# Kernel optimization log

Hardware: AMD Instinct MI355X
Metric: run time of the kernel (lower is better)

Reference implementation:

```python
import jax, jax.numpy as jnp
import numpy as np

N, D_MODEL, D_PE, H = 4096, 512, 16, 8


def setup_inputs() -> dict:
    key = jax.random.key(0)
    ks = jax.random.split(key, 6)
    s = 1.0 / np.sqrt(D_MODEL)
    return {
        "x": jax.random.normal(ks[0], (N, D_MODEL), dtype=jnp.float32),
        "pe": jax.random.normal(ks[1], (N, D_PE), dtype=jnp.float32),
        "w_qkv": jax.random.normal(ks[2], (D_MODEL, 3 * D_MODEL), dtype=jnp.float32) * s,
        "b_qkv": jnp.zeros((3 * D_MODEL,), dtype=jnp.float32),
        "w_pe": jax.random.normal(ks[3], (D_PE, H), dtype=jnp.float32) * (1.0 / np.sqrt(D_PE)),
        "b_pe": jnp.zeros((H,), dtype=jnp.float32),
        "w_out": jax.random.normal(ks[4], (D_MODEL, D_MODEL), dtype=jnp.float32) * s,
        "b_out": jnp.zeros((D_MODEL,), dtype=jnp.float32),
    }


def reference(x, pe, w_qkv, b_qkv, w_pe, b_pe, w_out, b_out):
    n, d = x.shape
    h = w_pe.shape[1]
    hd = d // h
    scale = hd ** -0.5

    qkv = (x @ w_qkv + b_qkv).reshape(n, 3, h, hd)  # [N,3,H,hd]
    q = jnp.transpose(qkv[:, 0], (1, 0, 2))  # [H,N,hd]
    k = jnp.transpose(qkv[:, 1], (1, 0, 2))
    v = jnp.transpose(qkv[:, 2], (1, 0, 2))

    pe_proj = pe @ w_pe + b_pe  # [N,H]
    # bias[h,i,j] = pe_proj[j,h] - pe_proj[i,h]  (matches torch unsqueeze/permute)
    pt = pe_proj.T  # [H,N]
    bias = pt[:, None, :] - pt[:, :, None]  # [H,N,N]

    scores = jnp.einsum('hnd,hmd->hnm', q, k) * scale + bias  # [H,N,N]
    attn = jax.nn.softmax(scores, axis=-1)
    out = jnp.einsum('hnm,hmd->hnd', attn, v)  # [H,N,hd]
    out = jnp.transpose(out, (1, 0, 2)).reshape(n, d)
    return out @ w_out + b_out
```

## Files before the change

### kernel.cpp

```cpp
#include <hip/hip_runtime.h>
#include <stdint.h>
#include <stddef.h>


typedef unsigned short u16;
typedef __attribute__((ext_vector_type(8))) short short8;
typedef __attribute__((ext_vector_type(8))) unsigned short us8;
typedef __attribute__((ext_vector_type(4))) unsigned short us4;
typedef __attribute__((ext_vector_type(4))) float floatx4;

__device__ __forceinline__ u16 f2b(float f) {
  union { float f; uint32_t u; } v; v.f = f;
  uint32_t u = v.u;
  return (u16)((u + 0x7fffu + ((u >> 16) & 1u)) >> 16);
}

__device__ __forceinline__ uint32_t pkbf16(float a, float b) {
  union { float f; uint32_t u; } x, y; x.f = a; y.f = b;
  return __builtin_amdgcn_perm(y.u + 0x8000u, x.u + 0x8000u, 0x07060302u);
}

#if __has_builtin(__builtin_amdgcn_exp2f)
__device__ __forceinline__ float fexp2(float x) { return __builtin_amdgcn_exp2f(x); }
#else
__device__ __forceinline__ float fexp2(float x) { return exp2f(x); }
#endif


__device__ __forceinline__ void tr_tile(const float* __restrict__ in,
                                        u16* __restrict__ out, int R, int C,
                                        int bx, int by, u16 (*tile)[33]) {
  int tx = threadIdx.x & 31, ty = threadIdx.x >> 5;
  int c0 = bx * 32, r0 = by * 32;
#pragma unroll
  for (int i = 0; i < 32; i += 8)
    tile[ty + i][tx] = f2b(in[(size_t)(r0 + ty + i) * C + c0 + tx]);
  __syncthreads();
#pragma unroll
  for (int i = 0; i < 32; i += 8)
    out[(size_t)(c0 + ty + i) * R + r0 + tx] = tile[tx][ty + i];
}

__global__ __launch_bounds__(256) void k_prep(
    const float* __restrict__ x, u16* __restrict__ xb,
    const float* __restrict__ w_qkv, u16* __restrict__ wqkvT,
    const float* __restrict__ w_out, u16* __restrict__ woutT,
    const float* __restrict__ pe, const float* __restrict__ w_pe,
    const float* __restrict__ b_pe, float* __restrict__ peT) {
  __shared__ u16 tile[32][33];
  int b = blockIdx.x;
  if (b < 2048) {
    int i = b * 256 + threadIdx.x;
    float4 v = ((const float4*)x)[i];
    uint2 o = make_uint2(pkbf16(v.x, v.y), pkbf16(v.z, v.w));
    ((uint2*)xb)[i] = o;
  } else if (b < 2816) {
    int idx = b - 2048;
    tr_tile(w_qkv, wqkvT, 512, 1536, idx % 48, idx / 48, tile);
  } else if (b < 3072) {
    int idx = b - 2816;
    tr_tile(w_out, woutT, 512, 512, idx % 16, idx / 16, tile);
  } else {
    int idx = (b - 3072) * 256 + threadIdx.x;
    int h = idx >> 12, n = idx & 4095;
    float acc = b_pe[h];
#pragma unroll
    for (int d = 0; d < 16; ++d) acc = fmaf(pe[n * 16 + d], w_pe[d * 8 + h], acc);
    peT[h * 4096 + n] = acc * 1.4426950408889634f - 16.0f;
  }
}


__global__ __launch_bounds__(256) void k_gemm_qkv(const u16* __restrict__ A,
                                                  const u16* __restrict__ Bt,
                                                  const float* __restrict__ bias,
                                                  u16* __restrict__ qk,
                                                  u16* __restrict__ vtp) {
  __shared__ u16 As[64 * 40];
  __shared__ u16 Bs[128 * 40];
  const int tid = threadIdx.x;
  const int lane = tid & 63, wave = tid >> 6;
  const int colx = lane & 15, quad = lane >> 4;
  const int m0 = blockIdx.y * 64, n0 = blockIdx.x * 128;
  const int wr = (wave >> 1) * 32, wc = (wave & 1) * 64;
  const floatx4 fz = {0.f, 0.f, 0.f, 0.f};
  floatx4 acc[2][4];
#pragma unroll
  for (int i = 0; i < 2; ++i)
#pragma unroll
    for (int j = 0; j < 4; ++j) acc[i][j] = fz;

  for (int k0 = 0; k0 < 512; k0 += 32) {
    __syncthreads();
    {
      int row = tid >> 2, ch = tid & 3;
      *(us8*)&As[row * 40 + ch * 8] =
          *(const us8*)&A[(size_t)(m0 + row) * 512 + k0 + ch * 8];
    }
#pragma unroll
    for (int r = 0; r < 2; ++r) {
      int idx = r * 256 + tid;
      int row = idx >> 2, ch = idx & 3;
      *(us8*)&Bs[row * 40 + ch * 8] =
          *(const us8*)&Bt[(size_t)(n0 + row) * 512 + k0 + ch * 8];
    }
    __syncthreads();
    short8 af[2], bf[4];
#pragma unroll
    for (int i = 0; i < 2; ++i)
      af[i] = *(const short8*)&As[(wr + i * 16 + colx) * 40 + quad * 8];
#pragma unroll
    for (int j = 0; j < 4; ++j)
      bf[j] = *(const short8*)&Bs[(wc + j * 16 + colx) * 40 + quad * 8];
#pragma unroll
    for (int i = 0; i < 2; ++i)
#pragma unroll
      for (int j = 0; j < 4; ++j)
        acc[i][j] = __builtin_amdgcn_mfma_f32_16x16x32_bf16(af[i], bf[j], acc[i][j], 0, 0, 0);
  }

  const bool isV = (blockIdx.x >= 8);
#pragma unroll
  for (int j = 0; j < 4; ++j) {
    int c = n0 + wc + j * 16 + colx;
    float bq = bias[c];
    if (!isV) {
#pragma unroll
      for (int i = 0; i < 2; ++i)
#pragma unroll
        for (int r = 0; r < 4; ++r) {
          int row = m0 + wr + i * 16 + quad * 4 + r;
          qk[(size_t)row * 1024 + c] = f2b(acc[i][j][r] + bq);
        }
    } else {
      int d = c - 1024;
#pragma unroll
      for (int i = 0; i < 2; ++i) {
        us4 o;
#pragma unroll
        for (int r = 0; r < 4; ++r) o[r] = f2b(acc[i][j][r] + bq);
        *(us4*)&vtp[(size_t)d * 4096 + m0 + wr + quad * 8 + i * 4] = o;
      }
    }
  }
}


__global__ __launch_bounds__(256) void k_gemm_out(const u16* __restrict__ A,
                                                  const u16* __restrict__ Bt,
                                                  const float* __restrict__ bias,
                                                  float* __restrict__ Cout) {
  __shared__ u16 As[64 * 40];
  __shared__ u16 Bs[64 * 40];
  const int tid = threadIdx.x;
  const int lane = tid & 63, wave = tid >> 6;
  const int colx = lane & 15, quad = lane >> 4;
  const int m0 = blockIdx.y * 64, n0 = blockIdx.x * 64;
  const int wr = (wave >> 1) * 32, wc = (wave & 1) * 32;
  const floatx4 fz = {0.f, 0.f, 0.f, 0.f};
  floatx4 acc[2][2];
#pragma unroll
  for (int i = 0; i < 2; ++i)
#pragma unroll
    for (int j = 0; j < 2; ++j) acc[i][j] = fz;

  for (int k0 = 0; k0 < 512; k0 += 32) {
    __syncthreads();
    {
      int row = tid >> 2, ch = tid & 3;
      *(us8*)&As[row * 40 + ch * 8] =
          *(const us8*)&A[(size_t)(m0 + row) * 512 + k0 + ch * 8];
      *(us8*)&Bs[row * 40 + ch * 8] =
          *(const us8*)&Bt[(size_t)(n0 + row) * 512 + k0 + ch * 8];
    }
    __syncthreads();
    short8 af[2], bf[2];
#pragma unroll
    for (int i = 0; i < 2; ++i)
      af[i] = *(const short8*)&As[(wr + i * 16 + colx) * 40 + quad * 8];
#pragma unroll
    for (int j = 0; j < 2; ++j)
      bf[j] = *(const short8*)&Bs[(wc + j * 16 + colx) * 40 + quad * 8];
#pragma unroll
    for (int i = 0; i < 2; ++i)
#pragma unroll
      for (int j = 0; j < 2; ++j)
        acc[i][j] = __builtin_amdgcn_mfma_f32_16x16x32_bf16(af[i], bf[j], acc[i][j], 0, 0, 0);
  }
#pragma unroll
  for (int j = 0; j < 2; ++j) {
    int c = n0 + wc + j * 16 + colx;
    float bq = bias[c];
#pragma unroll
    for (int i = 0; i < 2; ++i)
#pragma unroll
      for (int r = 0; r < 4; ++r) {
        int row = m0 + wr + i * 16 + quad * 4 + r;
        Cout[(size_t)row * 512 + c] = acc[i][j][r] + bq;
      }
  }
}


__global__ __launch_bounds__(512, 4) void k_flash(const u16* __restrict__ qk,
                                                  const u16* __restrict__ vt,
                                                  const float* __restrict__ peT,
                                                  u16* __restrict__ ao) {
  __shared__ __align__(16) u16 smem[18176];
  u16* Ks = smem;
  u16* Vts = smem + 9216;
  float* pes = (float*)(smem + 17920);
  float* bufs = (float*)smem;
  u16* fin = smem;

  const int tid = threadIdx.x;
  const int lane = tid & 63, wave = tid >> 6;
  const int colx = lane & 15, quad = lane >> 4;
  const int ih = wave & 1, jq = wave >> 1;
  const int q0 = blockIdx.x * 64;
  const int h = blockIdx.y;
  const float sscale = 0.125f * 1.4426950408889634f;
  const floatx4 fz = {0.f, 0.f, 0.f, 0.f};

  {
    int row = tid >> 3, ch = tid & 7;
    *(us8*)&Ks[row * 72 + ch * 8] =
        *(const us8*)&qk[(size_t)(q0 + row) * 1024 + h * 64 + ch * 8];
  }
  __syncthreads();
  short8 qf[2][2];
#pragma unroll
  for (int i2 = 0; i2 < 2; ++i2)
#pragma unroll
    for (int kk = 0; kk < 2; ++kk)
      qf[i2][kk] = *(const short8*)&Ks[(ih * 32 + i2 * 16 + colx) * 72 + kk * 32 + quad * 8];

  floatx4 oacc[2][4];
  float rsum[2] = {0.0f, 0.0f};
#pragma unroll
  for (int i2 = 0; i2 < 2; ++i2)
#pragma unroll
    for (int cb = 0; cb < 4; ++cb) oacc[i2][cb] = fz;

  for (int j0 = 0; j0 < 4096; j0 += 128) {
    __syncthreads();
#pragma unroll
    for (int r = 0; r < 2; ++r) {
      int idx = r * 512 + tid;
      int row = idx >> 3, ch = idx & 7;
      *(us8*)&Ks[row * 72 + ch * 8] =
          *(const us8*)&qk[(size_t)(j0 + row) * 1024 + 512 + h * 64 + ch * 8];
    }
#pragma unroll
    for (int r = 0; r < 2; ++r) {
      int idx = r * 512 + tid;
      int row = idx >> 4, ch = idx & 15;
      *(us8*)&Vts[row * 136 + ch * 8] =
          *(const us8*)&vt[(size_t)(h * 64 + row) * 4096 + j0 + ch * 8];
    }
    if (tid < 128) pes[tid] = peT[h * 4096 + j0 + tid];
    __syncthreads();

    short8 kf[2][2];
#pragma unroll
    for (int j2 = 0; j2 < 2; ++j2)
#pragma unroll
      for (int kk = 0; kk < 2; ++kk)
        kf[j2][kk] = *(const short8*)&Ks[(jq * 32 + j2 * 16 + colx) * 72 + kk * 32 + quad * 8];
    short8 vf[4];
#pragma unroll
    for (int cb = 0; cb < 4; ++cb)
      vf[cb] = *(const short8*)&Vts[(cb * 16 + colx) * 136 + jq * 32 + quad * 8];
    floatx4 pev[2];
#pragma unroll
    for (int j2 = 0; j2 < 2; ++j2)
      pev[j2] = *(const floatx4*)&pes[jq * 32 + j2 * 16 + quad * 4];

#pragma unroll
    for (int i2 = 0; i2 < 2; ++i2) {
      floatx4 sacc[2] = {fz, fz};
#pragma unroll
      for (int j2 = 0; j2 < 2; ++j2)
#pragma unroll
        for (int kk = 0; kk < 2; ++kk)
          sacc[j2] = __builtin_amdgcn_mfma_f32_16x16x32_bf16(kf[j2][kk], qf[i2][kk], sacc[j2], 0, 0, 0);
      union { uint32_t w[4]; short8 s; } pk;
#pragma unroll
      for (int j2 = 0; j2 < 2; ++j2) {
        float p0 = fexp2(fmaf(sacc[j2][0], sscale, pev[j2][0]));
        float p1 = fexp2(fmaf(sacc[j2][1], sscale, pev[j2][1]));
        float p2 = fexp2(fmaf(sacc[j2][2], sscale, pev[j2][2]));
        float p3 = fexp2(fmaf(sacc[j2][3], sscale, pev[j2][3]));
        rsum[i2] += (p0 + p1) + (p2 + p3);
        pk.w[j2 * 2 + 0] = pkbf16(p0, p1);
        pk.w[j2 * 2 + 1] = pkbf16(p2, p3);
      }
#pragma unroll
      for (int cb = 0; cb < 4; ++cb)
        oacc[i2][cb] = __builtin_amdgcn_mfma_f32_16x16x32_bf16(pk.s, vf[cb], oacc[i2][cb], 0, 0, 0);
    }
  }

  floatx4 lacc[2];
#pragma unroll
  for (int i2 = 0; i2 < 2; ++i2) {
    rsum[i2] += __shfl_xor(rsum[i2], 16);
    rsum[i2] += __shfl_xor(rsum[i2], 32);
#pragma unroll
    for (int r = 0; r < 4; ++r) lacc[i2][r] = __shfl(rsum[i2], quad * 4 + r, 16);
  }

  __syncthreads();
  float* s0 = bufs + (0 * 2 + ih) * 2080;
  float* s1 = bufs + (1 * 2 + ih) * 2080;
  if (jq >= 2) {
    float* b = (jq == 2) ? s0 : s1;
#pragma unroll
    for (int i2 = 0; i2 < 2; ++i2) {
#pragma unroll
      for (int cb = 0; cb < 4; ++cb)
#pragma unroll
        for (int r = 0; r < 4; ++r)
          b[(i2 * 16 + quad * 4 + r) * 65 + cb * 16 + colx] = oacc[i2][cb][r];
      if (colx == 0)
#pragma unroll
        for (int r = 0; r < 4; ++r)
          b[(i2 * 16 + quad * 4 + r) * 65 + 64] = lacc[i2][r];
    }
  }
  __syncthreads();
  if (jq < 2) {
    float* b = (jq == 0) ? s0 : s1;
#pragma unroll
    for (int i2 = 0; i2 < 2; ++i2) {
#pragma unroll
      for (int cb = 0; cb < 4; ++cb)
#pragma unroll
        for (int r = 0; r < 4; ++r)
          oacc[i2][cb][r] += b[(i2 * 16 + quad * 4 + r) * 65 + cb * 16 + colx];
#pragma unroll
      for (int r = 0; r < 4; ++r)
        lacc[i2][r] += b[(i2 * 16 + quad * 4 + r) * 65 + 64];
    }
  }
  __syncthreads();
  if (jq == 1) {
#pragma unroll
    for (int i2 = 0; i2 < 2; ++i2) {
#pragma unroll
      for (int cb = 0; cb < 4; ++cb)
#pragma unroll
        for (int r = 0; r < 4; ++r)
          s1[(i2 * 16 + quad * 4 + r) * 65 + cb * 16 + colx] = oacc[i2][cb][r];
      if (colx == 0)
#pragma unroll
        for (int r = 0; r < 4; ++r)
          s1[(i2 * 16 + quad * 4 + r) * 65 + 64] = lacc[i2][r];
    }
  }
  __syncthreads();
  if (jq == 0) {
#pragma unroll
    for (int i2 = 0; i2 < 2; ++i2) {
#pragma unroll
      for (int cb = 0; cb < 4; ++cb)
#pragma unroll
        for (int r = 0; r < 4; ++r)
          oacc[i2][cb][r] += s1[(i2 * 16 + quad * 4 + r) * 65 + cb * 16 + colx];
#pragma unroll
      for (int r = 0; r < 4; ++r)
        lacc[i2][r] += s1[(i2 * 16 + quad * 4 + r) * 65 + 64];
#pragma unroll
      for (int r = 0; r < 4; ++r) {
        float inv = 1.0f / lacc[i2][r];
#pragma unroll
        for (int cb = 0; cb < 4; ++cb)
          fin[(ih * 32 + i2 * 16 + quad * 4 + r) * 68 + cb * 16 + colx] =
              f2b(oacc[i2][cb][r] * inv);
      }
    }
  }
  __syncthreads();
  {
    int row = tid >> 3, ch = tid & 7;
    *(us8*)&ao[(size_t)(q0 + row) * 512 + h * 64 + ch * 8] =
        *(const us8*)&fin[row * 68 + ch * 8];
  }
}


extern "C" void kernel_launch(void* const* d_in, const int* in_sizes, int n_in,
                              void* d_out, int out_size, void* d_ws, size_t ws_size,
                              hipStream_t stream) {
  const float* x     = (const float*)d_in[0];
  const float* pe    = (const float*)d_in[1];
  const float* w_qkv = (const float*)d_in[2];
  const float* b_qkv = (const float*)d_in[3];
  const float* w_pe  = (const float*)d_in[4];
  const float* b_pe  = (const float*)d_in[5];
  const float* w_out = (const float*)d_in[6];
  const float* b_out = (const float*)d_in[7];
  float* out = (float*)d_out;

  u16* xb    = (u16*)d_ws;
  u16* wqkvT = xb    + 2097152;
  u16* woutT = wqkvT + 786432;
  u16* qk    = woutT + 262144;
  u16* vt    = qk    + 4194304;
  u16* ao    = vt    + 2097152;
  float* peT = (float*)(ao + 2097152);

  k_prep<<<3200, 256, 0, stream>>>(x, xb, w_qkv, wqkvT, w_out, woutT,
                                   pe, w_pe, b_pe, peT);
  k_gemm_qkv<<<dim3(12, 64), 256, 0, stream>>>(xb, wqkvT, b_qkv, qk, vt);
  k_flash<<<dim3(64, 8), 512, 0, stream>>>(qk, vt, peT, ao);
  k_gemm_out<<<dim3(8, 64), 256, 0, stream>>>(ao, woutT, b_out, out);
}
```

Baseline: 155.8 us.

## Double-buffer GEMM and flash tiles via direct global-to-LDS loads with XOR swizzle

```diff
diff --git a/kernel.cpp b/kernel.cpp
--- a/kernel.cpp
+++ b/kernel.cpp
@@ -25,6 +25,12 @@
 #else
 __device__ __forceinline__ float fexp2(float x) { return exp2f(x); }
 #endif
+
+__device__ __forceinline__ void gld16(const u16* g, u16* l) {
+  __builtin_amdgcn_global_load_lds(
+      (const __attribute__((address_space(1))) uint32_t*)(const void*)g,
+      (__attribute__((address_space(3))) uint32_t*)(void*)l, 16, 0, 0);
+}
 
 
 __device__ __forceinline__ void tr_tile(const float* __restrict__ in,
@@ -76,13 +82,14 @@
                                                   const float* __restrict__ bias,
                                                   u16* __restrict__ qk,
                                                   u16* __restrict__ vtp) {
-  __shared__ u16 As[64 * 40];
-  __shared__ u16 Bs[128 * 40];
+  __shared__ __align__(16) u16 smem[12288];
   const int tid = threadIdx.x;
   const int lane = tid & 63, wave = tid >> 6;
   const int colx = lane & 15, quad = lane >> 4;
   const int m0 = blockIdx.y * 64, n0 = blockIdx.x * 128;
   const int wr = (wave >> 1) * 32, wc = (wave & 1) * 64;
+  const int scA = (lane & 3) ^ ((lane >> 3) & 3);
+  const int sx = (colx >> 1) & 3;
   const floatx4 fz = {0.f, 0.f, 0.f, 0.f};
   floatx4 acc[2][4];
 #pragma unroll
@@ -90,33 +97,38 @@
 #pragma unroll
     for (int j = 0; j < 4; ++j) acc[i][j] = fz;
 
-  for (int k0 = 0; k0 < 512; k0 += 32) {
-    __syncthreads();
-    {
-      int row = tid >> 2, ch = tid & 3;
-      *(us8*)&As[row * 40 + ch * 8] =
-          *(const us8*)&A[(size_t)(m0 + row) * 512 + k0 + ch * 8];
-    }
-#pragma unroll
-    for (int r = 0; r < 2; ++r) {
-      int idx = r * 256 + tid;
-      int row = idx >> 2, ch = idx & 3;
-      *(us8*)&Bs[row * 40 + ch * 8] =
-          *(const us8*)&Bt[(size_t)(n0 + row) * 512 + k0 + ch * 8];
-    }
-    __syncthreads();
+#define PREF_QKV(k0, b)                                                       \
+  {                                                                           \
+    int rowa = wave * 16 + (lane >> 2);                                       \
+    gld16(&A[(size_t)(m0 + rowa) * 512 + (k0) + scA * 8],                     \
+          &smem[(b) * 2048 + wave * 512 + lane * 8]);                         \
+    _Pragma("unroll") for (int c = 0; c < 2; ++c) {                           \
+      int rowb = wave * 32 + c * 16 + (lane >> 2);                            \
+      gld16(&Bt[(size_t)(n0 + rowb) * 512 + (k0) + scA * 8],                  \
+            &smem[4096 + (b) * 4096 + wave * 1024 + c * 512 + lane * 8]);     \
+    }                                                                         \
+  }
+
+  PREF_QKV(0, 0);
+  __syncthreads();
+  for (int it = 0; it < 16; ++it) {
+    int cur = it & 1;
+    if (it < 15) PREF_QKV((it + 1) * 32, cur ^ 1);
+    const u16* As = &smem[cur * 2048];
+    const u16* Bs = &smem[4096 + cur * 4096];
     short8 af[2], bf[4];
 #pragma unroll
     for (int i = 0; i < 2; ++i)
-      af[i] = *(const short8*)&As[(wr + i * 16 + colx) * 40 + quad * 8];
+      af[i] = *(const short8*)&As[(wr + i * 16 + colx) * 32 + (quad ^ sx) * 8];
 #pragma unroll
     for (int j = 0; j < 4; ++j)
-      bf[j] = *(const short8*)&Bs[(wc + j * 16 + colx) * 40 + quad * 8];
+      bf[j] = *(const short8*)&Bs[(wc + j * 16 + colx) * 32 + (quad ^ sx) * 8];
 #pragma unroll
     for (int i = 0; i < 2; ++i)
 #pragma unroll
       for (int j = 0; j < 4; ++j)
         acc[i][j] = __builtin_amdgcn_mfma_f32_16x16x32_bf16(af[i], bf[j], acc[i][j], 0, 0, 0);
+    __syncthreads();
   }
 
   const bool isV = (blockIdx.x >= 8);
@@ -143,6 +155,7 @@
       }
     }
   }
+#undef PREF_QKV
 }
 
 
@@ -150,13 +163,14 @@
                                                   const u16* __restrict__ Bt,
                                                   const float* __restrict__ bias,
                                                   float* __restrict__ Cout) {
-  __shared__ u16 As[64 * 40];
-  __shared__ u16 Bs[64 * 40];
+  __shared__ __align__(16) u16 smem[8192];
   const int tid = threadIdx.x;
   const int lane = tid & 63, wave = tid >> 6;
   const int colx = lane & 15, quad = lane >> 4;
   const int m0 = blockIdx.y * 64, n0 = blockIdx.x * 64;
   const int wr = (wave >> 1) * 32, wc = (wave & 1) * 32;
+  const int scA = (lane & 3) ^ ((lane >> 3) & 3);
+  const int sx = (colx >> 1) & 3;
   const floatx4 fz = {0.f, 0.f, 0.f, 0.f};
   floatx4 acc[2][2];
 #pragma unroll
@@ -164,28 +178,35 @@
 #pragma unroll
     for (int j = 0; j < 2; ++j) acc[i][j] = fz;
 
-  for (int k0 = 0; k0 < 512; k0 += 32) {
-    __syncthreads();
-    {
-      int row = tid >> 2, ch = tid & 3;
-      *(us8*)&As[row * 40 + ch * 8] =
-          *(const us8*)&A[(size_t)(m0 + row) * 512 + k0 + ch * 8];
-      *(us8*)&Bs[row * 40 + ch * 8] =
-          *(const us8*)&Bt[(size_t)(n0 + row) * 512 + k0 + ch * 8];
-    }
-    __syncthreads();
+#define PREF_OUT(k0, b)                                                       \
+  {                                                                           \
+    int rowa = wave * 16 + (lane >> 2);                                       \
+    gld16(&A[(size_t)(m0 + rowa) * 512 + (k0) + scA * 8],                     \
+          &smem[(b) * 2048 + wave * 512 + lane * 8]);                         \
+    gld16(&Bt[(size_t)(n0 + rowa) * 512 + (k0) + scA * 8],                    \
+          &smem[4096 + (b) * 2048 + wave * 512 + lane * 8]);                  \
+  }
+
+  PREF_OUT(0, 0);
+  __syncthreads();
+  for (int it = 0; it < 16; ++it) {
+    int cur = it & 1;
+    if (it < 15) PREF_OUT((it + 1) * 32, cur ^ 1);
+    const u16* As = &smem[cur * 2048];
+    const u16* Bs = &smem[4096 + cur * 2048];
     short8 af[2], bf[2];
 #pragma unroll
     for (int i = 0; i < 2; ++i)
-      af[i] = *(const short8*)&As[(wr + i * 16 + colx) * 40 + quad * 8];
+      af[i] = *(const short8*)&As[(wr + i * 16 + colx) * 32 + (quad ^ sx) * 8];
 #pragma unroll
     for (int j = 0; j < 2; ++j)
-      bf[j] = *(const short8*)&Bs[(wc + j * 16 + colx) * 40 + quad * 8];
+      bf[j] = *(const short8*)&Bs[(wc + j * 16 + colx) * 32 + (quad ^ sx) * 8];
 #pragma unroll
     for (int i = 0; i < 2; ++i)
 #pragma unroll
       for (int j = 0; j < 2; ++j)
         acc[i][j] = __builtin_amdgcn_mfma_f32_16x16x32_bf16(af[i], bf[j], acc[i][j], 0, 0, 0);
+    __syncthreads();
   }
 #pragma unroll
   for (int j = 0; j < 2; ++j) {
@@ -199,6 +220,7 @@
         Cout[(size_t)row * 512 + c] = acc[i][j][r] + bq;
       }
   }
+#undef PREF_OUT
 }
 
 
@@ -206,10 +228,7 @@
                                                   const u16* __restrict__ vt,
                                                   const float* __restrict__ peT,
                                                   u16* __restrict__ ao) {
-  __shared__ __align__(16) u16 smem[18176];
-  u16* Ks = smem;
-  u16* Vts = smem + 9216;
-  float* pes = (float*)(smem + 17920);
+  __shared__ __align__(16) u16 smem[37376];
   float* bufs = (float*)smem;
   u16* fin = smem;
 
@@ -222,18 +241,43 @@
   const float sscale = 0.125f * 1.4426950408889634f;
   const floatx4 fz = {0.f, 0.f, 0.f, 0.f};
 
+  const int scK = (lane & 7) ^ (lane >> 3);
+  const int rV = wave * 8 + (lane >> 4);
+  const int scV0 = (lane & 15) ^ (rV & 15);
+  const int scV1 = (lane & 15) ^ ((rV + 4) & 15);
+
+#define PREF_F(j0n, b)                                                        \
+  {                                                                           \
+    _Pragma("unroll") for (int c = 0; c < 2; ++c) {                           \
+      int row = wave * 16 + c * 8 + (lane >> 3);                              \
+      gld16(&qk[(size_t)((j0n) + row) * 1024 + 512 + h * 64 + scK * 8],       \
+            &smem[4096 + (b) * 8192 + wave * 1024 + c * 512 + lane * 8]);     \
+    }                                                                         \
+    gld16(&vt[(size_t)(h * 64 + rV) * 4096 + (j0n) + scV0 * 8],               \
+          &smem[20480 + (b) * 8192 + wave * 1024 + lane * 8]);                \
+    gld16(&vt[(size_t)(h * 64 + rV + 4) * 4096 + (j0n) + scV1 * 8],           \
+          &smem[20480 + (b) * 8192 + wave * 1024 + 512 + lane * 8]);          \
+    if (tid < 128)                                                            \
+      ((float*)(smem + 36864 + (b) * 256))[tid] = peT[h * 4096 + (j0n) + tid];\
+  }
+
   {
     int row = tid >> 3, ch = tid & 7;
-    *(us8*)&Ks[row * 72 + ch * 8] =
+    int slot = ch ^ (row & 7);
+    *(us8*)&smem[row * 64 + slot * 8] =
         *(const us8*)&qk[(size_t)(q0 + row) * 1024 + h * 64 + ch * 8];
   }
-  __syncthreads();
+  PREF_F(0, 0);
+  __syncthreads();
+
   short8 qf[2][2];
 #pragma unroll
   for (int i2 = 0; i2 < 2; ++i2)
 #pragma unroll
-    for (int kk = 0; kk < 2; ++kk)
-      qf[i2][kk] = *(const short8*)&Ks[(ih * 32 + i2 * 16 + colx) * 72 + kk * 32 + quad * 8];
+    for (int kk = 0; kk < 2; ++kk) {
+      int row = ih * 32 + i2 * 16 + colx;
+      qf[i2][kk] = *(const short8*)&smem[row * 64 + ((kk * 4 + quad) ^ (colx & 7)) * 8];
+    }
 
   floatx4 oacc[2][4];
   float rsum[2] = {0.0f, 0.0f};
@@ -242,35 +286,28 @@
 #pragma unroll
     for (int cb = 0; cb < 4; ++cb) oacc[i2][cb] = fz;
 
-  for (int j0 = 0; j0 < 4096; j0 += 128) {
-    __syncthreads();
-#pragma unroll
-    for (int r = 0; r < 2; ++r) {
-      int idx = r * 512 + tid;
-      int row = idx >> 3, ch = idx & 7;
-      *(us8*)&Ks[row * 72 + ch * 8] =
-          *(const us8*)&qk[(size_t)(j0 + row) * 1024 + 512 + h * 64 + ch * 8];
-    }
-#pragma unroll
-    for (int r = 0; r < 2; ++r) {
-      int idx = r * 512 + tid;
-      int row = idx >> 4, ch = idx & 15;
-      *(us8*)&Vts[row * 136 + ch * 8] =
-          *(const us8*)&vt[(size_t)(h * 64 + row) * 4096 + j0 + ch * 8];
-    }
-    if (tid < 128) pes[tid] = peT[h * 4096 + j0 + tid];
-    __syncthreads();
+  for (int it = 0; it < 32; ++it) {
+    const int cur = it & 1;
+    if (it < 31) PREF_F((it + 1) * 128, cur ^ 1);
+
+    const u16* Ks = &smem[4096 + cur * 8192];
+    const u16* Vts = &smem[20480 + cur * 8192];
+    const float* pes = (const float*)(smem + 36864 + cur * 256);
 
     short8 kf[2][2];
 #pragma unroll
     for (int j2 = 0; j2 < 2; ++j2)
 #pragma unroll
-      for (int kk = 0; kk < 2; ++kk)
-        kf[j2][kk] = *(const short8*)&Ks[(jq * 32 + j2 * 16 + colx) * 72 + kk * 32 + quad * 8];
+      for (int kk = 0; kk < 2; ++kk) {
+        int row = jq * 32 + j2 * 16 + colx;
+        kf[j2][kk] = *(const short8*)&Ks[row * 64 + ((kk * 4 + quad) ^ (colx & 7)) * 8];
+      }
     short8 vf[4];
 #pragma unroll
-    for (int cb = 0; cb < 4; ++cb)
-      vf[cb] = *(const short8*)&Vts[(cb * 16 + colx) * 136 + jq * 32 + quad * 8];
+    for (int cb = 0; cb < 4; ++cb) {
+      int row = cb * 16 + colx;
+      vf[cb] = *(const short8*)&Vts[row * 128 + ((jq * 4 + quad) ^ colx) * 8];
+    }
     floatx4 pev[2];
 #pragma unroll
     for (int j2 = 0; j2 < 2; ++j2)
@@ -299,6 +336,7 @@
       for (int cb = 0; cb < 4; ++cb)
         oacc[i2][cb] = __builtin_amdgcn_mfma_f32_16x16x32_bf16(pk.s, vf[cb], oacc[i2][cb], 0, 0, 0);
     }
+    __syncthreads();
   }
 
   floatx4 lacc[2];
@@ -310,7 +348,6 @@
     for (int r = 0; r < 4; ++r) lacc[i2][r] = __shfl(rsum[i2], quad * 4 + r, 16);
   }
 
-  __syncthreads();
   float* s0 = bufs + (0 * 2 + ih) * 2080;
   float* s1 = bufs + (1 * 2 + ih) * 2080;
   if (jq >= 2) {
@@ -386,6 +423,7 @@
     *(us8*)&ao[(size_t)(q0 + row) * 512 + h * 64 + ch * 8] =
         *(const us8*)&fin[row * 68 + ch * 8];
   }
+#undef PREF_F
 }
 
 
```

Result: faster. 149.2 us (-4.2%).
